# Kernel optimization log

Hardware: AMD Instinct MI355X
Metric: run time of the kernel (lower is better)

## Reference

```python
import jax, jax.numpy as jnp
import numpy as np
import math

H = 16          # n_head
N_EMBD = 1024
EPS = 1e-5      # torch LayerNorm default


def setup_inputs() -> dict:
    key = jax.random.key(0)
    ks = jax.random.split(key, 6)
    B, T, C = 2, 2048, 1024
    x = jax.random.normal(ks[0], (B, T, C), dtype=jnp.float32)
    s = 0.02  # GPT-2 style init scale keeps softmax logits sane
    Wq = jax.random.normal(ks[1], (C, N_EMBD), dtype=jnp.float32) * s
    Wk = jax.random.normal(ks[2], (C, N_EMBD), dtype=jnp.float32) * s
    Wv = jax.random.normal(ks[3], (C, N_EMBD), dtype=jnp.float32) * s
    Wo = jax.random.normal(ks[4], (N_EMBD, C), dtype=jnp.float32) * s
    return {
        "x": x,
        "Wq": Wq, "bq": jnp.zeros((N_EMBD,), jnp.float32),
        "Wk": Wk, "bk": jnp.zeros((N_EMBD,), jnp.float32),
        "Wv": Wv, "bv": jnp.zeros((N_EMBD,), jnp.float32),
        "Wo": Wo, "bo": jnp.zeros((C,), jnp.float32),
        "gamma": jnp.ones((C,), jnp.float32),
        "beta": jnp.zeros((C,), jnp.float32),
    }


def reference(x, Wq, bq, Wk, bk, Wv, bv, Wo, bo, gamma, beta):
    B, T, _ = x.shape
    Dh = N_EMBD // H
    # projections -> (B, H, T, Dh)
    def split_heads(y):
        return y.reshape(B, T, H, Dh).transpose(0, 2, 1, 3)
    q = split_heads(x @ Wq + bq)
    k = split_heads(x @ Wk + bk)
    v = split_heads(x @ Wv + bv)
    # naive causal attention: explicit (B,H,T,T) scores
    att = jnp.einsum("bhtd,bhsd->bhts", q, k) * (1.0 / math.sqrt(Dh))
    causal = jnp.tril(jnp.ones((T, T), dtype=bool))
    att = jnp.where(causal[None, None], att, -jnp.inf)
    att = jax.nn.softmax(att, axis=-1)
    o = jnp.einsum("bhts,bhsd->bhtd", att, v)
    o = o.transpose(0, 2, 1, 3).reshape(B, T, N_EMBD)
    y = o @ Wo + bo
    # LayerNorm (dropout is identity at p=0 / eval)
    mu = jnp.mean(y, axis=-1, keepdims=True)
    var = jnp.var(y, axis=-1, keepdims=True)
    return (y - mu) * jax.lax.rsqrt(var + EPS) * gamma + beta
```

## Files before the change

### kernel.cpp

```cpp
#include <hip/hip_runtime.h>
#include <stdint.h>
#include <stddef.h>

typedef __attribute__((ext_vector_type(8))) short short8;
typedef __attribute__((ext_vector_type(4))) float f32x4;
typedef __attribute__((ext_vector_type(16))) float f32x16;
typedef __attribute__((ext_vector_type(4))) unsigned short us4;
typedef __attribute__((ext_vector_type(4))) unsigned u32x4;

#define DEVI static __device__ __forceinline__

DEVI unsigned short f2bf(float f) {
  unsigned u = __builtin_bit_cast(unsigned, f);
  u += 0x7FFFu + ((u >> 16) & 1u);
  return (unsigned short)(u >> 16);
}

DEVI float bf2f(unsigned short u) {
  return __builtin_bit_cast(float, ((unsigned)u) << 16);
}

DEVI f32x4 mfma16(short8 a, short8 b, f32x4 c) {
  return __builtin_amdgcn_mfma_f32_16x16x32_bf16(a, b, c, 0, 0, 0);
}

DEVI f32x16 mfma32(short8 a, short8 b, f32x16 c) {
  return __builtin_amdgcn_mfma_f32_32x32x16_bf16(a, b, c, 0, 0, 0);
}

DEVI unsigned cvtpk(float lo, float hi) {
  unsigned r;
  asm("v_cvt_pk_bf16_f32 %0, %1, %2" : "=v"(r) : "v"(lo), "v"(hi));
  return r;
}

DEVI void plswap(unsigned& a, unsigned& b) {
  asm("v_permlane32_swap_b32 %0, %1" : "+v"(a), "+v"(b));
}

DEVI float ex2(float x) {
  float r;
  asm("v_exp_f32 %0, %1" : "=v"(r) : "v"(x));
  return r;
}

DEVI f32x16 zero16() {
  f32x16 z;
#pragma unroll
  for (int i = 0; i < 16; ++i) z[i] = 0.f;
  return z;
}

DEVI void glds16(const void* g, void* l) {
  __builtin_amdgcn_global_load_lds(
      (const __attribute__((address_space(1))) void*)g,
      (__attribute__((address_space(3))) void*)l, 16, 0, 0);
}

__global__ __launch_bounds__(256) void k_cvt_x(const float* __restrict__ x,
                                               unsigned short* __restrict__ xb) {
  size_t i = ((size_t)blockIdx.x * 256 + threadIdx.x) * 8;
  f32x4 a = *(const f32x4*)(x + i);
  f32x4 b = *(const f32x4*)(x + i + 4);
  short8 v;
#pragma unroll
  for (int j = 0; j < 4; ++j) {
    v[j] = (short)f2bf(a[j]);
    v[4 + j] = (short)f2bf(b[j]);
  }
  *(short8*)(xb + i) = v;
}

__global__ __launch_bounds__(256) void k_twT4(const float* __restrict__ W0,
                                              const float* __restrict__ W1,
                                              const float* __restrict__ W2,
                                              const float* __restrict__ W3,
                                              unsigned short* __restrict__ WT) {
  __shared__ float tile[64][65];
  const int z = blockIdx.z;
  const float* W = (z == 0) ? W0 : (z == 1) ? W1 : (z == 2) ? W2 : W3;
  unsigned short* out = WT + (size_t)z * 1024 * 1024;
  const int n0 = blockIdx.x * 64, k0 = blockIdx.y * 64;
  const int t = threadIdx.x, rr = t >> 4, cc = (t & 15) * 4;
#pragma unroll
  for (int i = 0; i < 4; ++i) {
    int row = i * 16 + rr;
    f32x4 v = *(const f32x4*)(W + (size_t)(k0 + row) * 1024 + n0 + cc);
#pragma unroll
    for (int j = 0; j < 4; ++j) tile[row][cc + j] = v[j];
  }
  __syncthreads();
#pragma unroll
  for (int i = 0; i < 4; ++i) {
    int nrow = i * 16 + rr;
    us4 u;
#pragma unroll
    for (int j = 0; j < 4; ++j) u[j] = f2bf(tile[cc + j][nrow]);
    *(us4*)(out + (size_t)(n0 + nrow) * 1024 + k0 + cc) = u;
  }
}

template <bool SWAP>
DEVI void gemm_core2(const unsigned short* __restrict__ A,
                     const unsigned short* __restrict__ Bt,
                     int mt, int nt, char* lds, f32x4 (&acc)[4][4]) {
  const int t = threadIdx.x;
  const int l = t & 63, c = l & 15, g = l >> 4;
  const int w = t >> 6, wr = w >> 1, wc = w & 1;
  const int srow = t >> 3;
  const int sxor = (((t & 7) ^ (srow & 7))) * 8;
  const unsigned short* Ab = A + (size_t)(mt * 128 + srow) * 1024 + sxor;
  const unsigned short* Bb = Bt + (size_t)(nt * 128 + srow) * 1024 + sxor;
  const int key = (c & 7);

  auto STAGE = [&](int kt, int buf) {
    char* lb = lds + buf * 32768;
#pragma unroll
    for (int i = 0; i < 4; ++i) {
      glds16(Ab + (size_t)i * 32 * 1024 + kt * 64, lb + i * 4096 + t * 16);
      glds16(Bb + (size_t)i * 32 * 1024 + kt * 64, lb + 16384 + i * 4096 + t * 16);
    }
  };

  STAGE(0, 0);
  asm volatile("s_waitcnt vmcnt(0)" ::: "memory");
  __builtin_amdgcn_s_barrier();
  asm volatile("" ::: "memory");
  for (int kt = 0; kt < 16; ++kt) {
    const int cur = kt & 1;
    if (kt < 15) STAGE(kt + 1, cur ^ 1);
    const char* lb = lds + cur * 32768;
#pragma unroll
    for (int ks = 0; ks < 2; ++ks) {
      short8 af[4], bfr[4];
#pragma unroll
      for (int m = 0; m < 4; ++m)
        af[m] = *(const short8*)(lb + (wr * 64 + m * 16 + c) * 128 +
                                 ((ks * 4 + g) ^ key) * 16);
#pragma unroll
      for (int n = 0; n < 4; ++n)
        bfr[n] = *(const short8*)(lb + 16384 + (wc * 64 + n * 16 + c) * 128 +
                                  ((ks * 4 + g) ^ key) * 16);
#pragma unroll
      for (int m = 0; m < 4; ++m)
#pragma unroll
        for (int n = 0; n < 4; ++n)
          acc[m][n] = SWAP ? mfma16(bfr[n], af[m], acc[m][n])
                           : mfma16(af[m], bfr[n], acc[m][n]);
    }
    asm volatile("s_waitcnt vmcnt(0)" ::: "memory");
    __builtin_amdgcn_s_barrier();
    asm volatile("" ::: "memory");
  }
}

DEVI void gemm_core5(const unsigned short* __restrict__ A,
                     const unsigned short* __restrict__ Bt,
                     int mt, int pt, char* lds, f32x4 (&acc)[8][3]) {
  const int t = threadIdx.x;
  const int l = t & 63, c = l & 15, g = l >> 4;
  const int w = t >> 6, wm = w >> 2, wn = w & 3;
  const int srow = t >> 3;
  const int sxor = ((t & 7) ^ (srow & 7)) * 8;
  const unsigned short* Ab = A + (size_t)(mt * 256 + srow) * 1024 + sxor;
  const unsigned short* Bb = Bt + (size_t)(pt * 192 + srow) * 1024 + sxor;
  const int key = c & 7;

  auto STAGE = [&](int kt, int buf) {
    char* lb = lds + buf * 57344;
#pragma unroll
    for (int i = 0; i < 4; ++i)
      glds16(Ab + (size_t)(i * 64) * 1024 + kt * 64, lb + i * 8192 + t * 16);
#pragma unroll
    for (int i = 0; i < 3; ++i)
      glds16(Bb + (size_t)(i * 64) * 1024 + kt * 64, lb + 32768 + i * 8192 + t * 16);
  };

  STAGE(0, 0);
  asm volatile("s_waitcnt vmcnt(0)" ::: "memory");
  __builtin_amdgcn_s_barrier();
  asm volatile("" ::: "memory");
  for (int kt = 0; kt < 16; ++kt) {
    const int cur = kt & 1;
    if (kt < 15) STAGE(kt + 1, cur ^ 1);
    const char* la = lds + cur * 57344;
    const char* lbB = la + 32768;
    short8 bf[3][2];
#pragma unroll
    for (int fc = 0; fc < 3; ++fc)
#pragma unroll
      for (int ks = 0; ks < 2; ++ks) {
        int brow = wn * 48 + fc * 16 + c;
        bf[fc][ks] = *(const short8*)(lbB + brow * 128 + (((ks * 4 + g) ^ key) * 16));
      }
#pragma unroll
    for (int p = 0; p < 4; ++p) {
      short8 af[2][2];
#pragma unroll
      for (int r2 = 0; r2 < 2; ++r2)
#pragma unroll
        for (int ks = 0; ks < 2; ++ks) {
          int arow = wm * 128 + (2 * p + r2) * 16 + c;
          af[r2][ks] = *(const short8*)(la + arow * 128 + (((ks * 4 + g) ^ key) * 16));
        }
      __builtin_amdgcn_s_setprio(1);
#pragma unroll
      for (int ks = 0; ks < 2; ++ks)
#pragma unroll
        for (int r2 = 0; r2 < 2; ++r2)
#pragma unroll
          for (int fc = 0; fc < 3; ++fc)
            acc[2 * p + r2][fc] = mfma16(bf[fc][ks], af[r2][ks], acc[2 * p + r2][fc]);
      __builtin_amdgcn_s_setprio(0);
    }
    asm volatile("s_waitcnt vmcnt(0)" ::: "memory");
    __builtin_amdgcn_s_barrier();
    asm volatile("" ::: "memory");
  }
}

__global__ __launch_bounds__(512) void k_gemm_qkv3(
    const unsigned short* __restrict__ A,
    const unsigned short* __restrict__ Wf,
    const float* __restrict__ b0, const float* __restrict__ b1, const float* __restrict__ b2,
    unsigned short* __restrict__ O0, unsigned short* __restrict__ O1,
    unsigned short* __restrict__ O2) {
  extern __shared__ char lds[];
  const int mt = blockIdx.x, pt = blockIdx.y;
  f32x4 acc[8][3];
#pragma unroll
  for (int m = 0; m < 8; ++m)
#pragma unroll
    for (int n = 0; n < 3; ++n) acc[m][n] = (f32x4){0.f, 0.f, 0.f, 0.f};
  gemm_core5(A, Wf, mt, pt, lds, acc);
  const int t = threadIdx.x, l = t & 63, c = l & 15, g = l >> 4;
  const int w = t >> 6, wm = w >> 2, wn = w & 3;
#pragma unroll
  for (int fc = 0; fc < 3; ++fc) {
    int colg3 = pt * 192 + wn * 48 + fc * 16 + 4 * g;
    int z = colg3 >> 10, colc = colg3 & 1023;
    const float* bias = (z == 0) ? b0 : (z == 1) ? b1 : b2;
    f32x4 bv4 = *(const f32x4*)(bias + colc);
    int h = colc >> 6, d = colc & 63;
    if (z < 2) {
      unsigned short* out = (z == 0) ? O0 : O1;
      const float sc = (z == 0) ? 0.18033688011f : 1.0f;
#pragma unroll
      for (int fr = 0; fr < 8; ++fr) {
        int rowg = mt * 256 + wm * 128 + fr * 16 + c;
        int b = rowg >> 11, tt = rowg & 2047;
        us4 u;
#pragma unroll
        for (int r = 0; r < 4; ++r) u[r] = f2bf((acc[fr][fc][r] + bv4[r]) * sc);
        *(us4*)(out + ((size_t)(b * 16 + h) * 2048 + tt) * 64 + d) = u;
      }
    } else {
#pragma unroll
      for (int fr = 0; fr < 8; ++fr) {
        int rowg = mt * 256 + wm * 128 + fr * 16 + c;
        int b = rowg >> 11, tt = rowg & 2047;
        size_t base = ((size_t)(b * 16 + h) * 64 + d) * 2048 + tt;
#pragma unroll
        for (int r = 0; r < 4; ++r)
          O2[base + (size_t)r * 2048] = f2bf(acc[fr][fc][r] + bv4[r]);
      }
    }
  }
}

__global__ __launch_bounds__(256) void k_gemm_proj(const unsigned short* __restrict__ A,
                                                   const unsigned short* __restrict__ Bt,
                                                   const float* __restrict__ bias,
                                                   unsigned short* __restrict__ Yb) {
  __shared__ char lds[65536];
  f32x4 acc[4][4];
#pragma unroll
  for (int m = 0; m < 4; ++m)
#pragma unroll
    for (int n = 0; n < 4; ++n) acc[m][n] = (f32x4){0.f, 0.f, 0.f, 0.f};
  const int lin = blockIdx.y * 32 + blockIdx.x;
  const int nt = lin & 7, mt = lin >> 3;
  gemm_core2<true>(A, Bt, mt, nt, lds, acc);
  const int t = threadIdx.x, l = t & 63, c = l & 15, g = l >> 4;
  const int w = t >> 6, wr = w >> 1, wc = w & 1;
#pragma unroll
  for (int n = 0; n < 4; ++n) {
    int colb = nt * 128 + wc * 64 + n * 16 + 4 * g;
    f32x4 bv4 = *(const f32x4*)(bias + colb);
#pragma unroll
    for (int m = 0; m < 4; ++m) {
      int rowg = mt * 128 + wr * 64 + m * 16 + c;
      us4 u;
#pragma unroll
      for (int r = 0; r < 4; ++r) u[r] = f2bf(acc[m][n][r] + bv4[r]);
      *(us4*)(Yb + (size_t)rowg * 1024 + colb) = u;
    }
  }
}

__global__ __launch_bounds__(256) void k_attn10(const unsigned short* __restrict__ Q,
                                                const unsigned short* __restrict__ K,
                                                const unsigned short* __restrict__ VT,
                                                unsigned short* __restrict__ O,
                                                unsigned short* __restrict__ P,
                                                float* __restrict__ ML) {
  __shared__ char lds[49152];
  const int bid = blockIdx.x;
  int qt, c0, NT, mode, bh;
  if (bid < 256) {
    mode = 1; qt = 8 + (bid >> 5); c0 = 0; NT = 16; bh = bid & 31;
  } else {
    int rem = bid - 256;
    int lvl = rem >> 6;
    int sub = rem & 63;
    bh = sub & 31;
    if (sub < 32) { mode = 0; qt = 7 - lvl;  c0 = 0;  NT = 2 * qt + 2; }
    else          { mode = 2; qt = 15 - lvl; c0 = 16; NT = 2 * qt - 14; }
  }
  const int t = threadIdx.x;
  const int w = t >> 6, l = t & 63;
  const int lq = l & 31, hi = l >> 5;
  const int q0 = qt * 128 + w * 32;
  const size_t kbase = (size_t)bh * 2048 * 64;
  const size_t vbase = (size_t)bh * 64 * 2048;
  const int srow = t >> 3;
  const int sx = ((t & 7) ^ (srow & 7)) * 8;
  const int my_nt = (mode == 1) ? 16 : (2 * qt + 1 + (w >> 1) - c0);

  short8 qf[4];
#pragma unroll
  for (int ds = 0; ds < 4; ++ds)
    qf[ds] = *(const short8*)(Q + kbase + (size_t)(q0 + lq) * 64 + 16 * ds + 8 * hi);

  auto STAGE = [&](int ktg, int buf) {
    const unsigned short* Kt = K + kbase + (size_t)ktg * 4096;
    const unsigned short* Vt = VT + vbase + ktg * 64;
    char* lb = lds + buf * 16384;
#pragma unroll
    for (int i = 0; i < 2; ++i) {
      int row = i * 32 + srow;
      glds16(Kt + (size_t)row * 64 + sx, lb + i * 4096 + t * 16);
      glds16(Vt + (size_t)row * 2048 + sx, lb + 8192 + i * 4096 + t * 16);
    }
  };

  f32x16 oacc[2];
  oacc[0] = zero16();
  oacc[1] = zero16();
  float l_s = 0.f;
  const int rx = lq & 7;

  STAGE(c0, 0);
  STAGE(c0 + 1, 1);
  asm volatile("s_waitcnt vmcnt(4)" ::: "memory");
  __builtin_amdgcn_s_barrier();
  asm volatile("" ::: "memory");
  for (int kt = 0; kt < NT; ++kt) {
    if (kt + 2 < NT) STAGE(c0 + kt + 2, (kt + 2) % 3);
    if (kt < my_nt) {
      const char* lb = lds + (kt % 3) * 16384;
      const int kv0 = (c0 + kt) * 64;
      short8 kf0[4], kf1[4];
#pragma unroll
      for (int ds = 0; ds < 4; ++ds) {
        int blk = ((ds * 2 + hi) ^ rx) * 16;
        kf0[ds] = *(const short8*)(lb + lq * 128 + blk);
        kf1[ds] = *(const short8*)(lb + (lq + 32) * 128 + blk);
      }
      f32x16 st0 = zero16(), st1 = zero16();
      __builtin_amdgcn_s_setprio(1);
#pragma unroll
      for (int ds = 0; ds < 4; ++ds) {
        st0 = mfma32(kf0[ds], qf[ds], st0);
        st1 = mfma32(kf1[ds], qf[ds], st1);
      }
      __builtin_amdgcn_s_setprio(0);
      short8 vf[2][4];
#pragma unroll
      for (int fd = 0; fd < 2; ++fd) {
        int d = fd * 32 + lq;
#pragma unroll
        for (int s = 0; s < 4; ++s)
          vf[fd][s] = *(const short8*)(lb + 8192 + d * 128 + (((s * 2 + hi) ^ rx) * 16));
      }
      if (mode != 1 && kt == my_nt - 1) {
        const int qg = q0 + lq;
#pragma unroll
        for (int r = 0; r < 16; ++r) {
          int kr = kv0 + (r & 3) + 8 * (r >> 2) + 4 * hi;
          if (kr > qg) st0[r] = -1e30f;
          if (kr + 32 > qg) st1[r] = -1e30f;
        }
      }
      unsigned Wp[2][4][2];
      float gs[8];
#pragma unroll
      for (int f = 0; f < 2; ++f)
#pragma unroll
        for (int m4 = 0; m4 < 4; ++m4) {
          float p0 = ex2((f ? st1 : st0)[4 * m4 + 0]);
          float p1 = ex2((f ? st1 : st0)[4 * m4 + 1]);
          float p2 = ex2((f ? st1 : st0)[4 * m4 + 2]);
          float p3 = ex2((f ? st1 : st0)[4 * m4 + 3]);
          gs[f * 4 + m4] = (p0 + p1) + (p2 + p3);
          Wp[f][m4][0] = cvtpk(p0, p1);
          Wp[f][m4][1] = cvtpk(p2, p3);
        }
      l_s += ((gs[0] + gs[1]) + (gs[2] + gs[3])) + ((gs[4] + gs[5]) + (gs[6] + gs[7]));
      __builtin_amdgcn_s_setprio(1);
#pragma unroll
      for (int s = 0; s < 4; ++s) {
        const int f = s >> 1, s2 = s & 1;
        unsigned a0 = Wp[f][2 * s2][0], b0 = Wp[f][2 * s2 + 1][0];
        unsigned a1 = Wp[f][2 * s2][1], b1 = Wp[f][2 * s2 + 1][1];
        plswap(a0, b0);
        plswap(a1, b1);
        u32x4 pw = {a0, a1, b0, b1};
        short8 pf = __builtin_bit_cast(short8, pw);
        oacc[0] = mfma32(vf[0][s], pf, oacc[0]);
        oacc[1] = mfma32(vf[1][s], pf, oacc[1]);
      }
      __builtin_amdgcn_s_setprio(0);
    }
    if (kt + 2 < NT) {
      asm volatile("s_waitcnt vmcnt(4)" ::: "memory");
    } else {
      asm volatile("s_waitcnt vmcnt(0)" ::: "memory");
    }
    __builtin_amdgcn_s_barrier();
    asm volatile("" ::: "memory");
  }
  l_s += __shfl_xor(l_s, 32, 64);
  if (mode == 0) {
    const float inv = 1.0f / l_s;
    const int b = bh >> 4, h = bh & 15;
    unsigned short* orow = O + ((size_t)b * 2048 + q0 + lq) * 1024 + h * 64 + 4 * hi;
#pragma unroll
    for (int f = 0; f < 2; ++f)
#pragma unroll
      for (int m4 = 0; m4 < 4; ++m4) {
        us4 u;
#pragma unroll
        for (int rr = 0; rr < 4; ++rr) u[rr] = f2bf(oacc[f][4 * m4 + rr] * inv);
        *(us4*)(orow + f * 32 + m4 * 8) = u;
      }
  } else {
    const int pid = ((qt - 8) * 32 + bh) * 2 + (mode - 1);
    const int row = w * 32 + lq;
    unsigned short* prow = P + (size_t)pid * 8192 + row * 64 + 4 * hi;
#pragma unroll
    for (int f = 0; f < 2; ++f)
#pragma unroll
      for (int m4 = 0; m4 < 4; ++m4) {
        us4 u;
#pragma unroll
        for (int rr = 0; rr < 4; ++rr) u[rr] = f2bf(oacc[f][4 * m4 + rr]);
        *(us4*)(prow + f * 32 + m4 * 8) = u;
      }
    if (hi == 0) {
      ML[pid * 256 + row] = 0.f;
      ML[pid * 256 + 128 + row] = l_s;
    }
  }
}

__global__ __launch_bounds__(128) void k_merge(const unsigned short* __restrict__ P,
                                               const float* __restrict__ ML,
                                               unsigned short* __restrict__ O) {
  const int blk = blockIdx.x;
  const int qt = 8 + (blk >> 5), bh = blk & 31;
  const int pidA = ((qt - 8) * 32 + bh) * 2, pidB = pidA + 1;
  const int r = threadIdx.x;
  float mA = ML[pidA * 256 + r], lA = ML[pidA * 256 + 128 + r];
  float mB = ML[pidB * 256 + r], lB = ML[pidB * 256 + 128 + r];
  float mM = fmaxf(mA, mB);
  float wA = ex2(mA - mM), wB = ex2(mB - mM);
  float inv = 1.f / (lA * wA + lB * wB);
  wA *= inv;
  wB *= inv;
  const unsigned short* pa = P + (size_t)pidA * 8192 + r * 64;
  const unsigned short* pb = P + (size_t)pidB * 8192 + r * 64;
  const int b = bh >> 4, h = bh & 15, q = qt * 128 + r;
  unsigned short* orow = O + ((size_t)b * 2048 + q) * 1024 + h * 64;
#pragma unroll
  for (int j = 0; j < 8; ++j) {
    short8 a = *(const short8*)(pa + j * 8);
    short8 c = *(const short8*)(pb + j * 8);
    short8 o;
#pragma unroll
    for (int k = 0; k < 8; ++k)
      o[k] = (short)f2bf(bf2f((unsigned short)a[k]) * wA +
                         bf2f((unsigned short)c[k]) * wB);
    *(short8*)(orow + j * 8) = o;
  }
}

__global__ __launch_bounds__(256) void k_ln(const unsigned short* __restrict__ Yb,
                                            const float* __restrict__ gamma,
                                            const float* __restrict__ beta,
                                            float* __restrict__ out) {
  __shared__ float red[8];
  const int row = blockIdx.x, t = threadIdx.x, w = t >> 6, l = t & 63;
  us4 vb = *(const us4*)(Yb + (size_t)row * 1024 + t * 4);
  f32x4 v;
#pragma unroll
  for (int j = 0; j < 4; ++j) v[j] = bf2f(vb[j]);
  float s = v[0] + v[1] + v[2] + v[3];
  float ss = v[0] * v[0] + v[1] * v[1] + v[2] * v[2] + v[3] * v[3];
#pragma unroll
  for (int d = 1; d < 64; d <<= 1) {
    s += __shfl_xor(s, d, 64);
    ss += __shfl_xor(ss, d, 64);
  }
  if (l == 0) {
    red[w] = s;
    red[4 + w] = ss;
  }
  __syncthreads();
  s = red[0] + red[1] + red[2] + red[3];
  ss = red[4] + red[5] + red[6] + red[7];
  float mean = s * (1.f / 1024.f);
  float var = ss * (1.f / 1024.f) - mean * mean;
  float rstd = rsqrtf(var + 1e-5f);
  f32x4 gv = *(const f32x4*)(gamma + t * 4);
  f32x4 bv = *(const f32x4*)(beta + t * 4);
  f32x4 ov;
#pragma unroll
  for (int j = 0; j < 4; ++j) ov[j] = (v[j] - mean) * rstd * gv[j] + bv[j];
  *(f32x4*)(out + (size_t)row * 1024 + t * 4) = ov;
}

extern "C" void kernel_launch(void* const* d_in, const int* in_sizes, int n_in,
                              void* d_out, int out_size, void* d_ws, size_t ws_size,
                              hipStream_t stream) {
  (void)in_sizes; (void)n_in; (void)out_size; (void)ws_size;
  const float* x = (const float*)d_in[0];
  const float* Wq = (const float*)d_in[1];
  const float* bq = (const float*)d_in[2];
  const float* Wk = (const float*)d_in[3];
  const float* bk = (const float*)d_in[4];
  const float* Wv = (const float*)d_in[5];
  const float* bv = (const float*)d_in[6];
  const float* Wo = (const float*)d_in[7];
  const float* bo = (const float*)d_in[8];
  const float* gamma = (const float*)d_in[9];
  const float* beta = (const float*)d_in[10];
  char* ws = (char*)d_ws;
  const size_t MB = 1024 * 1024;
  unsigned short* xb = (unsigned short*)(ws);
  unsigned short* WT = (unsigned short*)(ws + 8 * MB);
  unsigned short* WoT = (unsigned short*)(ws + 14 * MB);
  unsigned short* Qb = (unsigned short*)(ws + 16 * MB);
  unsigned short* Kb = (unsigned short*)(ws + 24 * MB);
  unsigned short* VTb = (unsigned short*)(ws + 32 * MB);
  unsigned short* Ob = (unsigned short*)(ws + 40 * MB);
  unsigned short* Yb = (unsigned short*)(ws + 16 * MB);
  unsigned short* Pp = (unsigned short*)(ws);
  float* MLp = (float*)(ws + 8 * MB);

  k_cvt_x<<<2048, 256, 0, stream>>>(x, xb);
  k_twT4<<<dim3(16, 16, 4), 256, 0, stream>>>(Wq, Wk, Wv, Wo, WT);
  k_gemm_qkv3<<<dim3(16, 16), 512, 114688, stream>>>(xb, WT, bq, bk, bv, Qb, Kb, VTb);
  k_attn10<<<768, 256, 0, stream>>>(Qb, Kb, VTb, Ob, Pp, MLp);
  k_merge<<<256, 128, 0, stream>>>(Pp, MLp, Ob);
  k_gemm_proj<<<dim3(32, 8), 256, 0, stream>>>(Ob, WoT, bo, Yb);
  k_ln<<<4096, 256, 0, stream>>>(Yb, gamma, beta, (float*)d_out);
}
```

Measured before the change: 107.4 us.

## Use 256x256 QKV tiles with staggered slab prefetch and vectorized V-transpose stores

The QKV projection GEMM changes from 256x192 tiles on a 16x16 grid to 256x256 tiles on a 12x16 grid. Each block now produces output for a single one of Q, K or V. Next-tile loads are split into slabs issued across the four inner sub-steps, with partial vmcnt waits and barriers, instead of one bulk prefetch followed by a full wait. For V, the MFMA operands are swapped so the transposed output can be written as 4-wide vector stores rather than scalar strided stores. The cost is 128KB of LDS per block, more barriers per k-step, and 192 blocks, which underfills the 256 CUs.

```diff
diff --git a/kernel.cpp b/kernel.cpp
--- a/kernel.cpp
+++ b/kernel.cpp
@@ -154,97 +154,108 @@
   }
 }
 
-DEVI void gemm_core5(const unsigned short* __restrict__ A,
+template <bool SWAP>
+DEVI void gemm_core8(const unsigned short* __restrict__ A,
                      const unsigned short* __restrict__ Bt,
-                     int mt, int pt, char* lds, f32x4 (&acc)[8][3]) {
+                     int mt, int ntz, char* lds, f32x4 (&acc)[8][4]) {
   const int t = threadIdx.x;
   const int l = t & 63, c = l & 15, g = l >> 4;
   const int w = t >> 6, wm = w >> 2, wn = w & 3;
   const int srow = t >> 3;
   const int sxor = ((t & 7) ^ (srow & 7)) * 8;
   const unsigned short* Ab = A + (size_t)(mt * 256 + srow) * 1024 + sxor;
-  const unsigned short* Bb = Bt + (size_t)(pt * 192 + srow) * 1024 + sxor;
+  const unsigned short* Bb = Bt + (size_t)(ntz * 256 + srow) * 1024 + sxor;
   const int key = c & 7;
 
-  auto STAGE = [&](int kt, int buf) {
-    char* lb = lds + buf * 57344;
-#pragma unroll
-    for (int i = 0; i < 4; ++i)
-      glds16(Ab + (size_t)(i * 64) * 1024 + kt * 64, lb + i * 8192 + t * 16);
-#pragma unroll
-    for (int i = 0; i < 3; ++i)
-      glds16(Bb + (size_t)(i * 64) * 1024 + kt * 64, lb + 32768 + i * 8192 + t * 16);
+  auto SLAB = [&](int kt, int buf, int which) {
+    char* dst = lds + buf * 65536 + which * 8192 + t * 16;
+    if (which < 4)
+      glds16(Ab + (size_t)(which * 64) * 1024 + kt * 64, dst);
+    else
+      glds16(Bb + (size_t)((which - 4) * 64) * 1024 + kt * 64, dst);
   };
 
-  STAGE(0, 0);
+#pragma unroll
+  for (int s = 0; s < 8; ++s) SLAB(0, 0, s);
   asm volatile("s_waitcnt vmcnt(0)" ::: "memory");
   __builtin_amdgcn_s_barrier();
   asm volatile("" ::: "memory");
+
   for (int kt = 0; kt < 16; ++kt) {
-    const int cur = kt & 1;
-    if (kt < 15) STAGE(kt + 1, cur ^ 1);
-    const char* la = lds + cur * 57344;
+    const char* la = lds + (kt & 1) * 65536;
     const char* lbB = la + 32768;
-    short8 bf[3][2];
-#pragma unroll
-    for (int fc = 0; fc < 3; ++fc)
-#pragma unroll
-      for (int ks = 0; ks < 2; ++ks) {
-        int brow = wn * 48 + fc * 16 + c;
-        bf[fc][ks] = *(const short8*)(lbB + brow * 128 + (((ks * 4 + g) ^ key) * 16));
-      }
+    const int nb = (kt + 1) & 1;
+    const bool pre = (kt + 1 < 16);
+    if (pre) { SLAB(kt + 1, nb, 4); SLAB(kt + 1, nb, 5); }
+    short8 bf[4][2];
+#pragma unroll
+    for (int fc = 0; fc < 4; ++fc)
+#pragma unroll
+      for (int ks = 0; ks < 2; ++ks)
+        bf[fc][ks] = *(const short8*)(lbB + (wn * 64 + fc * 16 + c) * 128 +
+                                      (((ks * 4 + g) ^ key) * 16));
 #pragma unroll
     for (int p = 0; p < 4; ++p) {
+      if (p == 1 && pre) { SLAB(kt + 1, nb, 6); SLAB(kt + 1, nb, 7); }
+      if (p == 2 && pre) { SLAB(kt + 1, nb, 0); SLAB(kt + 1, nb, 2); }
+      if (p == 3 && pre) { SLAB(kt + 1, nb, 1); SLAB(kt + 1, nb, 3); }
       short8 af[2][2];
 #pragma unroll
       for (int r2 = 0; r2 < 2; ++r2)
 #pragma unroll
-        for (int ks = 0; ks < 2; ++ks) {
-          int arow = wm * 128 + (2 * p + r2) * 16 + c;
-          af[r2][ks] = *(const short8*)(la + arow * 128 + (((ks * 4 + g) ^ key) * 16));
-        }
+        for (int ks = 0; ks < 2; ++ks)
+          af[r2][ks] = *(const short8*)(la + (wm * 128 + p * 32 + r2 * 16 + c) * 128 +
+                                        (((ks * 4 + g) ^ key) * 16));
       __builtin_amdgcn_s_setprio(1);
 #pragma unroll
       for (int ks = 0; ks < 2; ++ks)
 #pragma unroll
         for (int r2 = 0; r2 < 2; ++r2)
 #pragma unroll
-          for (int fc = 0; fc < 3; ++fc)
-            acc[2 * p + r2][fc] = mfma16(bf[fc][ks], af[r2][ks], acc[2 * p + r2][fc]);
+          for (int fc = 0; fc < 4; ++fc)
+            acc[p * 2 + r2][fc] = SWAP
+                ? mfma16(bf[fc][ks], af[r2][ks], acc[p * 2 + r2][fc])
+                : mfma16(af[r2][ks], bf[fc][ks], acc[p * 2 + r2][fc]);
       __builtin_amdgcn_s_setprio(0);
-    }
-    asm volatile("s_waitcnt vmcnt(0)" ::: "memory");
-    __builtin_amdgcn_s_barrier();
-    asm volatile("" ::: "memory");
-  }
-}
-
-__global__ __launch_bounds__(512) void k_gemm_qkv3(
+      if (p == 1) {
+        if (pre) asm volatile("s_waitcnt vmcnt(4)" ::: "memory");
+        else     asm volatile("s_waitcnt vmcnt(0)" ::: "memory");
+      } else if (p == 3) {
+        if (pre) asm volatile("s_waitcnt vmcnt(2)" ::: "memory");
+        else     asm volatile("s_waitcnt vmcnt(0)" ::: "memory");
+      }
+      __builtin_amdgcn_s_barrier();
+      asm volatile("" ::: "memory");
+    }
+  }
+}
+
+__global__ __launch_bounds__(512) void k_gemm_qkv5(
     const unsigned short* __restrict__ A,
     const unsigned short* __restrict__ Wf,
     const float* __restrict__ b0, const float* __restrict__ b1, const float* __restrict__ b2,
     unsigned short* __restrict__ O0, unsigned short* __restrict__ O1,
     unsigned short* __restrict__ O2) {
   extern __shared__ char lds[];
-  const int mt = blockIdx.x, pt = blockIdx.y;
-  f32x4 acc[8][3];
+  const int ntz = blockIdx.x, mt = blockIdx.y;
+  const int z = ntz >> 2, ntl = ntz & 3;
+  const float* bias = (z == 0) ? b0 : (z == 1) ? b1 : b2;
+  f32x4 acc[8][4];
 #pragma unroll
   for (int m = 0; m < 8; ++m)
 #pragma unroll
-    for (int n = 0; n < 3; ++n) acc[m][n] = (f32x4){0.f, 0.f, 0.f, 0.f};
-  gemm_core5(A, Wf, mt, pt, lds, acc);
+    for (int n = 0; n < 4; ++n) acc[m][n] = (f32x4){0.f, 0.f, 0.f, 0.f};
   const int t = threadIdx.x, l = t & 63, c = l & 15, g = l >> 4;
   const int w = t >> 6, wm = w >> 2, wn = w & 3;
-#pragma unroll
-  for (int fc = 0; fc < 3; ++fc) {
-    int colg3 = pt * 192 + wn * 48 + fc * 16 + 4 * g;
-    int z = colg3 >> 10, colc = colg3 & 1023;
-    const float* bias = (z == 0) ? b0 : (z == 1) ? b1 : b2;
-    f32x4 bv4 = *(const f32x4*)(bias + colc);
-    int h = colc >> 6, d = colc & 63;
-    if (z < 2) {
+  if (z < 2) {
+    gemm_core8<true>(A, Wf, mt, ntz, lds, acc);
+    const float sc = (z == 0) ? 0.18033688011f : 1.0f;
+#pragma unroll
+    for (int fc = 0; fc < 4; ++fc) {
+      int colc = ntl * 256 + wn * 64 + fc * 16 + 4 * g;
+      f32x4 bv4 = *(const f32x4*)(bias + colc);
+      int h = colc >> 6, d = colc & 63;
       unsigned short* out = (z == 0) ? O0 : O1;
-      const float sc = (z == 0) ? 0.18033688011f : 1.0f;
 #pragma unroll
       for (int fr = 0; fr < 8; ++fr) {
         int rowg = mt * 256 + wm * 128 + fr * 16 + c;
@@ -254,15 +265,22 @@
         for (int r = 0; r < 4; ++r) u[r] = f2bf((acc[fr][fc][r] + bv4[r]) * sc);
         *(us4*)(out + ((size_t)(b * 16 + h) * 2048 + tt) * 64 + d) = u;
       }
-    } else {
+    }
+  } else {
+    gemm_core8<false>(A, Wf, mt, ntz, lds, acc);
+#pragma unroll
+    for (int fc = 0; fc < 4; ++fc) {
+      int colg = ntl * 256 + wn * 64 + fc * 16 + c;
+      float bvv = bias[colg];
+      int h = colg >> 6, d = colg & 63;
 #pragma unroll
       for (int fr = 0; fr < 8; ++fr) {
-        int rowg = mt * 256 + wm * 128 + fr * 16 + c;
+        int rowg = mt * 256 + wm * 128 + fr * 16 + 4 * g;
         int b = rowg >> 11, tt = rowg & 2047;
-        size_t base = ((size_t)(b * 16 + h) * 64 + d) * 2048 + tt;
-#pragma unroll
-        for (int r = 0; r < 4; ++r)
-          O2[base + (size_t)r * 2048] = f2bf(acc[fr][fc][r] + bv4[r]);
+        us4 u;
+#pragma unroll
+        for (int r = 0; r < 4; ++r) u[r] = f2bf(acc[fr][fc][r] + bvv);
+        *(us4*)(O2 + ((size_t)(b * 16 + h) * 64 + d) * 2048 + tt) = u;
       }
     }
   }
@@ -560,7 +578,7 @@
 
   k_cvt_x<<<2048, 256, 0, stream>>>(x, xb);
   k_twT4<<<dim3(16, 16, 4), 256, 0, stream>>>(Wq, Wk, Wv, Wo, WT);
-  k_gemm_qkv3<<<dim3(16, 16), 512, 114688, stream>>>(xb, WT, bq, bk, bv, Qb, Kb, VTb);
+  k_gemm_qkv5<<<dim3(12, 16), 512, 131072, stream>>>(xb, WT, bq, bk, bv, Qb, Kb, VTb);
   k_attn10<<<768, 256, 0, stream>>>(Qb, Kb, VTb, Ob, Pp, MLp);
   k_merge<<<256, 128, 0, stream>>>(Pp, MLp, Ob);
   k_gemm_proj<<<dim3(32, 8), 256, 0, stream>>>(Ob, WoT, bo, Yb);
```

After: 111.5 us. 1.04x slower.
